# Kernel optimization log

Hardware: AMD Instinct MI355X
Metric: run time of the kernel (lower is better)

## Reference

```python
import jax, jax.numpy as jnp
import numpy as np

N = 100_000      # nodes
E = 3_200_000    # edges (avg degree 32)
F_IN = 100       # raw feature dim (embedding Linear(100, 64))
H = 64           # in/hidden/out channels
C = 18           # class_num
EPS = 1e-12      # F.normalize eps


def _sage_conv(x, src, dst, edge_weight, Wl, bl, Wr):
    """PyG-style SAGEConv: mean-aggregate neighbor messages, two linears, L2 normalize."""
    msg = x[src]                                   # [E, d] gather of x_j
    if edge_weight is not None:
        msg = msg * edge_weight[:, None]
    agg = jax.ops.segment_sum(msg, dst, num_segments=N)                       # [N, d]
    deg = jax.ops.segment_sum(jnp.ones((src.shape[0],), x.dtype), dst, num_segments=N)
    mean = agg / jnp.maximum(deg, 1.0)[:, None]
    out = mean @ Wl + bl + x @ Wr                  # lin_l(aggr) + lin_r(root)
    nrm = jnp.sqrt(jnp.sum(out * out, axis=-1, keepdims=True))
    return out / jnp.maximum(nrm, EPS)


def setup_inputs() -> dict:
    key = jax.random.key(0)
    ks = jax.random.split(key, 16)
    s = 0.1
    inp = {
        "x": jax.random.normal(ks[0], (N, F_IN), jnp.float32),
        "edge_index": jax.random.randint(ks[1], (2, E), 0, N, dtype=jnp.int64),
        "edge_weight": jax.random.uniform(ks[2], (E,), jnp.float32),
        "emb_W": jax.random.normal(ks[3], (F_IN, H), jnp.float32) * s,
        "emb_b": jnp.zeros((H,), jnp.float32),
    }
    k = 4
    for i in (1, 2, 3):
        inp[f"Wl{i}"] = jax.random.normal(ks[k], (H, H), jnp.float32) * s; k += 1
        inp[f"bl{i}"] = jnp.zeros((H,), jnp.float32)
        inp[f"Wr{i}"] = jax.random.normal(ks[k], (H, H), jnp.float32) * s; k += 1
    inp["Wl4"] = jax.random.normal(ks[k], (H, C), jnp.float32) * s; k += 1
    inp["bl4"] = jnp.zeros((C,), jnp.float32)
    inp["Wr4"] = jax.random.normal(ks[k], (H, C), jnp.float32) * s
    return inp


def reference(x, edge_index, edge_weight, emb_W, emb_b,
              Wl1, bl1, Wr1, Wl2, bl2, Wr2, Wl3, bl3, Wr3,
              Wl4, bl4, Wr4):
    src, dst = edge_index[0], edge_index[1]
    h = jax.nn.relu(x @ emb_W + emb_b)             # embedding MLP
    for Wl, bl, Wr in ((Wl1, bl1, Wr1), (Wl2, bl2, Wr2), (Wl3, bl3, Wr3)):
        h = jax.nn.relu(_sage_conv(h, src, dst, edge_weight, Wl, bl, Wr))
        # dropout p=0.2 is identity in eval mode
    return _sage_conv(h, src, dst, None, Wl4, bl4, Wr4)
```

## Files before the change

kernel.cpp:

```cpp
#include <hip/hip_runtime.h>
#include <hip/hip_bf16.h>

#define N_NODES   100000
#define N_EDGES   3200000
#define F_IN      100
#define H_DIM     64
#define C_NUM     18
#define NPB       256
#define N_BKT     391
#define EPB       8192
#define N_TILES   1563

typedef __attribute__((ext_vector_type(8))) short short8;
typedef __attribute__((ext_vector_type(4))) float f32x4;
typedef __attribute__((ext_vector_type(2))) float f32x2;

__device__ __forceinline__ float ldf(const void* p, long long i, int isbf) {
    if (isbf) return __bfloat162float(((const __hip_bfloat16*)p)[i]);
    return ((const float*)p)[i];
}
__device__ __forceinline__ int ldi(const void* p, long long i, int is64) {
    if (is64) return (int)(((const long long*)p)[i]);
    return ((const int*)p)[i];
}
__device__ __forceinline__ unsigned short f2us(float f) {
    __hip_bfloat16 b = __float2bfloat16(f);
    return *(unsigned short*)&b;
}
__device__ __forceinline__ unsigned char f2fp8(float f) {
    int p = __builtin_amdgcn_cvt_pk_fp8_f32(f, 0.0f, 0, false);
    return (unsigned char)(p & 0xFF);
}

__global__ void detect_kernel(const void* ei, const void* x, int* flags)
{
    if (blockIdx.x != 0 || threadIdx.x >= 64) return;
    const int lane = threadIdx.x;
    const long long* e64 = (const long long*)ei;
    int bad = 0;
#pragma unroll
    for (int i = lane; i < 128; i += 64) {
        long long v = e64[i];
        if (v < 0 || v >= N_NODES) bad = 1;
    }
    unsigned long long anybad = __ballot(bad);
    const __hip_bfloat16* xb = (const __hip_bfloat16*)x;
    int cnt = 0;
#pragma unroll
    for (int i = lane; i < 256; i += 64) {
        float v = fabsf(__bfloat162float(xb[i]));
        if (v == 0.0f || (v > 9.5367431640625e-7f && v < 1.0e6f)) ++cnt;
    }
#pragma unroll
    for (int m = 1; m <= 32; m <<= 1) cnt += __shfl_xor(cnt, m);
    if (lane == 0) {
        flags[0] = (anybad == 0ULL) ? 1 : 0;
        flags[1] = (cnt >= 240) ? 1 : 0;
    }
}

__global__ void zero_cnt(int* __restrict__ pcnt)
{
    int i = threadIdx.x;
    if (i < N_BKT) pcnt[i] = 0;
}

__global__ __launch_bounds__(1024) void radix_count(const void* ei, int* __restrict__ pcnt,
                                                    const int* __restrict__ flags)
{
    __shared__ int hist[N_BKT];
    const int t = threadIdx.x;
    if (t < N_BKT) hist[t] = 0;
    __syncthreads();
    const int base = blockIdx.x * EPB;
    const int n = min(EPB, N_EDGES - base);
    const int is64 = flags[0];
    for (int j = t; j < n; j += 1024) {
        int d = ldi(ei, (long long)N_EDGES + base + j, is64);
        atomicAdd(&hist[d >> 8], 1);
    }
    __syncthreads();
    if (t < N_BKT) atomicAdd(&pcnt[t], hist[t]);
}

__global__ void scan_bkt(const int* __restrict__ cnt, int* __restrict__ base,
                         int* __restrict__ cursor)
{
    __shared__ int tmp[512];
    const int t = threadIdx.x;
    int v = (t < N_BKT) ? cnt[t] : 0;
    tmp[t] = v;
    __syncthreads();
    for (int off = 1; off < 512; off <<= 1) {
        int add = (t >= off) ? tmp[t - off] : 0;
        __syncthreads();
        tmp[t] += add;
        __syncthreads();
    }
    if (t < N_BKT) { base[t] = tmp[t] - v; cursor[t] = tmp[t] - v; }
    if (t == 511) base[N_BKT] = tmp[511];
}

__global__ __launch_bounds__(1024) void radix_scatter(const void* ei, const void* ew,
                                                      int* __restrict__ gcursor,
                                                      uint2* __restrict__ temp,
                                                      const int* __restrict__ flags)
{
    __shared__ uint2 stage[EPB];
    __shared__ int hist[512], scan_s[512];
    __shared__ int gbase[N_BKT], lcur[N_BKT];
    const int t = threadIdx.x;
    if (t < 512) hist[t] = 0;
    __syncthreads();

    const int base = blockIdx.x * EPB;
    const int n = min(EPB, N_EDGES - base);
    const int is64 = flags[0], isbf = flags[1];

    int  bkt[8];
    uint2 pk[8];
#pragma unroll
    for (int j = 0; j < 8; ++j) {
        int i = j * 1024 + t;
        bkt[j] = -1;
        if (i < n) {
            int e = base + i;
            int s = ldi(ei, e, is64);
            int d = ldi(ei, (long long)N_EDGES + e, is64);
            float w = ldf(ew, e, isbf);
            bkt[j] = d >> 8;
            pk[j].x = (unsigned)s | ((unsigned)(d & (NPB - 1)) << 17);
            pk[j].y = (unsigned)f2us(w) | ((unsigned)bkt[j] << 16);
            atomicAdd(&hist[bkt[j]], 1);
        }
    }
    __syncthreads();
    if (t < 512) scan_s[t] = hist[t];
    __syncthreads();
    for (int off = 1; off < 512; off <<= 1) {
        int add = 0;
        if (t < 512 && t >= off) add = scan_s[t - off];
        __syncthreads();
        if (t < 512) scan_s[t] += add;
        __syncthreads();
    }
    if (t < N_BKT) {
        int excl = scan_s[t] - hist[t];
        lcur[t] = excl;
        gbase[t] = atomicAdd(&gcursor[t], hist[t]) - excl;
    }
    __syncthreads();
#pragma unroll
    for (int j = 0; j < 8; ++j) {
        if (bkt[j] >= 0) {
            int pos = atomicAdd(&lcur[bkt[j]], 1);
            stage[pos] = pk[j];
        }
    }
    __syncthreads();
#pragma unroll
    for (int j = 0; j < 8; ++j) {
        int i = j * 1024 + t;
        if (i < n) {
            int b = (int)(stage[i].y >> 16);
            temp[gbase[b] + i] = stage[i];
        }
    }
}

__global__ __launch_bounds__(256) void csr_build(const uint2* __restrict__ temp,
                          const int* __restrict__ pbase,
                          unsigned int* __restrict__ csr_pk,
                          int* __restrict__ deg, int* __restrict__ row_start,
                          float* __restrict__ inv_deg)
{
    __shared__ int cnt[NPB], scan_s[NPB], cur[NPB];
    const int b = blockIdx.x;
    const int t = threadIdx.x;
    cnt[t] = 0;
    __syncthreads();
    const int bs = pbase[b];
    const int be = pbase[b + 1];
    for (int i = bs + t; i < be; i += NPB)
        atomicAdd(&cnt[(temp[i].x >> 17) & (NPB - 1)], 1);
    __syncthreads();
    int v = cnt[t];
    scan_s[t] = v;
    __syncthreads();
    for (int off = 1; off < NPB; off <<= 1) {
        int add = (t >= off) ? scan_s[t - off] : 0;
        __syncthreads();
        scan_s[t] += add;
        __syncthreads();
    }
    int excl = bs + scan_s[t] - v;
    cur[t] = excl;
    int node = b * NPB + t;
    if (node < N_NODES) {
        deg[node]       = v;
        row_start[node] = excl;
        inv_deg[node]   = 1.0f / (float)max(v, 1);
    }
    __syncthreads();
    for (int i = bs + t; i < be; i += NPB) {
        uint2 e = temp[i];
        int k = (e.x >> 17) & (NPB - 1);
        int pos = atomicAdd(&cur[k], 1);
        csr_pk[pos] = (e.x & 0x1FFFFu) | ((e.y & 0x7FFFu) << 17);
    }
}

template <int CP, int COUT>
__device__ __forceinline__ void stage_W(unsigned short* W_s, const void* Wl, const void* Wr,
                                        int t, int isbf)
{
    constexpr int KP = 136;
    const int n0 = t >> 3, k8a = t & 7;
    for (int n = n0; n < CP; n += 32) {
#pragma unroll
        for (int hh = 0; hh < 2; ++hh) {
            int k8 = k8a + hh * 8;
            union { unsigned short u[8]; short8 v; } tmp;
#pragma unroll
            for (int j = 0; j < 8; ++j) {
                int k = k8 * 8 + j;
                float val = 0.0f;
                if (n < COUT && k < 128)
                    val = (k < 64) ? ldf(Wl, (long long)k * COUT + n, isbf)
                                   : ldf(Wr, (long long)(k - 64) * COUT + n, isbf);
                tmp.u[j] = f2us(val);
            }
            *(short8*)&W_s[n * KP + k8 * 8] = tmp.v;
        }
    }
}

__global__ void embed_mfma(const void* x, const void* W, const void* b,
                           __hip_bfloat16* __restrict__ h,
                           unsigned char* __restrict__ h8,
                           const int* __restrict__ flags)
{
    constexpr int KP = 136;
    __shared__ unsigned short W_s[H_DIM * KP];
    __shared__ unsigned short x_s[64 * KP];
    __shared__ float b_s[H_DIM];
    const int t = threadIdx.x;
    const int isbf = flags[1];

    {
        const int n0 = t >> 3, k8a = t & 7;
        for (int n = n0; n < H_DIM; n += 32) {
#pragma unroll
            for (int hh = 0; hh < 2; ++hh) {
                int k8 = k8a + hh * 8;
                union { unsigned short u[8]; short8 v; } tmp;
#pragma unroll
                for (int j = 0; j < 8; ++j) {
                    int k = k8 * 8 + j;
                    tmp.u[j] = (k < F_IN) ? f2us(ldf(W, (long long)k * H_DIM + n, isbf))
                                          : (unsigned short)0;
                }
                *(short8*)&W_s[n * KP + k8 * 8] = tmp.v;
            }
        }
    }
    if (t < H_DIM) b_s[t] = ldf(b, t, isbf);
    for (int i = t; i < 64 * 36; i += 256) {
        int row = i / 36, col = 100 + (i % 36);
        x_s[row * KP + col] = 0;
    }

    const int wave = t >> 6, lane = t & 63, c = lane & 15, quad = lane >> 4;

    for (int tile = blockIdx.x; tile < N_TILES; tile += gridDim.x) {
        const int nb0 = tile * 64;
        const int valid = min(64, N_NODES - nb0);
        __syncthreads();
        if (isbf) {
            const uint2* xu = (const uint2*)x + (size_t)nb0 * 25;
            for (int i2 = t; i2 < valid * 25; i2 += 256) {
                int row = i2 / 25, col4 = i2 - row * 25;
                *(uint2*)&x_s[row * KP + col4 * 4] = xu[i2];
            }
        } else {
            for (int i = t; i < valid * 100; i += 256) {
                int row = i / 100, col = i - row * 100;
                x_s[row * KP + col] = f2us(((const float*)x)[(size_t)(nb0 + row) * 100 + col]);
            }
        }
        if (valid < 64) {
            for (int i = t; i < (64 - valid) * 100; i += 256) {
                int row = valid + i / 100, col = i % 100;
                x_s[row * KP + col] = 0;
            }
        }
        __syncthreads();

        short8 bfrag[4][4];
#pragma unroll
        for (int nt = 0; nt < 4; ++nt)
#pragma unroll
            for (int kt = 0; kt < 4; ++kt)
                bfrag[nt][kt] = *(const short8*)&W_s[(nt * 16 + c) * KP + kt * 32 + quad * 8];

        short8 afrag[4];
#pragma unroll
        for (int kt = 0; kt < 4; ++kt)
            afrag[kt] = *(const short8*)&x_s[(wave * 16 + c) * KP + kt * 32 + quad * 8];

        f32x4 acc[4] = {};
#pragma unroll
        for (int nt = 0; nt < 4; ++nt)
#pragma unroll
            for (int kt = 0; kt < 4; ++kt)
                acc[nt] = __builtin_amdgcn_mfma_f32_16x16x32_bf16(afrag[kt], bfrag[nt][kt], acc[nt], 0, 0, 0);

        const int nb = nb0 + wave * 16;
#pragma unroll
        for (int nt = 0; nt < 4; ++nt)
#pragma unroll
            for (int reg = 0; reg < 4; ++reg) {
                int nn = nb + quad * 4 + reg;
                int col = nt * 16 + c;
                if (nn < N_NODES) {
                    float v = fmaxf(acc[nt][reg] + b_s[col], 0.0f);
                    h[(size_t)nn * H_DIM + col] = __float2bfloat16(v);
                    h8[(size_t)nn * H_DIM + col] = f2fp8(v);
                }
            }
    }
}

#define ACC16(HV, W) do {                                                          \
    f32x2 f_;                                                                      \
    f_ = __builtin_amdgcn_cvt_pk_f32_fp8((int)HV.x, false); a[0]=fmaf(W,f_.x,a[0]);  a[1]=fmaf(W,f_.y,a[1]);   \
    f_ = __builtin_amdgcn_cvt_pk_f32_fp8((int)HV.x, true ); a[2]=fmaf(W,f_.x,a[2]);  a[3]=fmaf(W,f_.y,a[3]);   \
    f_ = __builtin_amdgcn_cvt_pk_f32_fp8((int)HV.y, false); a[4]=fmaf(W,f_.x,a[4]);  a[5]=fmaf(W,f_.y,a[5]);   \
    f_ = __builtin_amdgcn_cvt_pk_f32_fp8((int)HV.y, true ); a[6]=fmaf(W,f_.x,a[6]);  a[7]=fmaf(W,f_.y,a[7]);   \
    f_ = __builtin_amdgcn_cvt_pk_f32_fp8((int)HV.z, false); a[8]=fmaf(W,f_.x,a[8]);  a[9]=fmaf(W,f_.y,a[9]);   \
    f_ = __builtin_amdgcn_cvt_pk_f32_fp8((int)HV.z, true ); a[10]=fmaf(W,f_.x,a[10]); a[11]=fmaf(W,f_.y,a[11]); \
    f_ = __builtin_amdgcn_cvt_pk_f32_fp8((int)HV.w, false); a[12]=fmaf(W,f_.x,a[12]); a[13]=fmaf(W,f_.y,a[13]); \
    f_ = __builtin_amdgcn_cvt_pk_f32_fp8((int)HV.w, true ); a[14]=fmaf(W,f_.x,a[14]); a[15]=fmaf(W,f_.y,a[15]); \
} while (0)

template <bool USE_W>
__global__ __launch_bounds__(256) void gather_mean(const unsigned char* __restrict__ h8,
                            const unsigned int* __restrict__ csr_pk,
                            const int* __restrict__ row_start,
                            const int* __restrict__ deg,
                            const float* __restrict__ inv_deg,
                            __hip_bfloat16* __restrict__ mean)
{
    const int lane = threadIdx.x & 63;
    const int c4 = lane & 3;
    const int r4 = lane >> 2;
    const int wid = blockIdx.x * 4 + (threadIdx.x >> 6);
    const int nw  = gridDim.x * 4;

    for (int n = wid; n < N_NODES; n += nw) {
        const int s0 = row_start[n];
        const int d0 = deg[n];
        unsigned int ev = (lane < d0) ? csr_pk[s0 + lane] : 0u;
        const int m0 = min(d0, 64);
        float a[16] = {};

        for (int j0 = 0; j0 < m0; j0 += 32) {
            unsigned int eA = __shfl(ev, j0 + r4);
            unsigned int eB = __shfl(ev, j0 + 16 + r4);
            uint4 hvA = *(const uint4*)(h8 + (size_t)(eA & 0x1FFFF) * H_DIM + 16 * c4);
            uint4 hvB = *(const uint4*)(h8 + (size_t)(eB & 0x1FFFF) * H_DIM + 16 * c4);
            float wA, wB;
            if (USE_W) {
                wA = __uint_as_float((eA & 0xFFFE0000u) >> 1);
                wB = __uint_as_float((eB & 0xFFFE0000u) >> 1);
            } else {
                wA = (j0 + r4 < m0) ? 1.0f : 0.0f;
                wB = (j0 + 16 + r4 < m0) ? 1.0f : 0.0f;
            }
            ACC16(hvA, wA);
            ACC16(hvB, wB);
        }
        for (int jb = 64; jb < d0; jb += 16) {
            int j = jb + r4;
            unsigned int e2 = (j < d0) ? csr_pk[s0 + j] : 0u;
            float w;
            if (USE_W) w = __uint_as_float((e2 & 0xFFFE0000u) >> 1);
            else       w = (j < d0) ? 1.0f : 0.0f;
            uint4 hv = *(const uint4*)(h8 + (size_t)(e2 & 0x1FFFF) * H_DIM + 16 * c4);
            ACC16(hv, w);
        }

#pragma unroll
        for (int i = 0; i < 8; ++i) {
            float keep = (lane & 4) ? a[i + 8] : a[i];
            float give = (lane & 4) ? a[i] : a[i + 8];
            a[i] = keep + __shfl_xor(give, 4);
        }
#pragma unroll
        for (int i = 0; i < 4; ++i) {
            float keep = (lane & 8) ? a[i + 4] : a[i];
            float give = (lane & 8) ? a[i] : a[i + 4];
            a[i] = keep + __shfl_xor(give, 8);
        }
#pragma unroll
        for (int i = 0; i < 2; ++i) {
            float keep = (lane & 16) ? a[i + 2] : a[i];
            float give = (lane & 16) ? a[i] : a[i + 2];
            a[i] = keep + __shfl_xor(give, 16);
        }
        {
            float keep = (lane & 32) ? a[1] : a[0];
            float give = (lane & 32) ? a[0] : a[1];
            a[0] = keep + __shfl_xor(give, 32);
        }
        const int f = c4 * 16 + ((lane >> 2) & 1) * 8 + ((lane >> 3) & 1) * 4
                    + ((lane >> 4) & 1) * 2 + ((lane >> 5) & 1);
        mean[(size_t)n * H_DIM + f] = __float2bfloat16(a[0] * inv_deg[n]);
    }
}

template <int COUT, bool RELU, bool FINAL>
__global__ void transform_mfma(const __hip_bfloat16* __restrict__ meanp,
                               const __hip_bfloat16* __restrict__ hp,
                               const void* Wl, const void* bl, const void* Wr,
                               __hip_bfloat16* __restrict__ h_out,
                               unsigned char* __restrict__ h8_out,
                               const int* __restrict__ flags, void* dout)
{
    constexpr int CP = (COUT + 15) & ~15;
    constexpr int NT = CP / 16;
    constexpr int KP = 136;
    __shared__ unsigned short W_s[CP * KP];
    __shared__ float b_s[CP];
    const int t = threadIdx.x;
    const int isbf = flags[1];
    stage_W<CP, COUT>(W_s, Wl, Wr, t, isbf);
    if (t < CP) b_s[t] = (t < COUT) ? ldf(bl, t, isbf) : 0.0f;
    __syncthreads();

    const int wave = t >> 6, lane = t & 63, c = lane & 15, quad = lane >> 4;
    short8 bfrag[NT][4];
#pragma unroll
    for (int nt = 0; nt < NT; ++nt)
#pragma unroll
        for (int kt = 0; kt < 4; ++kt)
            bfrag[nt][kt] = *(const short8*)&W_s[(nt * 16 + c) * KP + kt * 32 + quad * 8];

    for (int tile = blockIdx.x; tile < N_TILES; tile += gridDim.x) {
        const int nbw = tile * 64 + wave * 16;
        if (nbw >= N_NODES) continue;
        int node = nbw + c; if (node >= N_NODES) node = N_NODES - 1;

        short8 afrag[4];
#pragma unroll
        for (int kt = 0; kt < 4; ++kt) {
            const __hip_bfloat16* sp = (kt < 2) ? meanp : hp;
            afrag[kt] = *(const short8*)(sp + (size_t)node * H_DIM + (kt & 1) * 32 + quad * 8);
        }

        f32x4 acc[NT] = {};
#pragma unroll
        for (int nt = 0; nt < NT; ++nt)
#pragma unroll
            for (int kt = 0; kt < 4; ++kt)
                acc[nt] = __builtin_amdgcn_mfma_f32_16x16x32_bf16(afrag[kt], bfrag[nt][kt], acc[nt], 0, 0, 0);

        float rs[4];
#pragma unroll
        for (int reg = 0; reg < 4; ++reg) {
            float s2 = 0.f;
#pragma unroll
            for (int nt = 0; nt < NT; ++nt) {
                float v = acc[nt][reg] + b_s[nt * 16 + c];
                acc[nt][reg] = v;
                s2 += v * v;
            }
            s2 += __shfl_xor(s2, 1); s2 += __shfl_xor(s2, 2);
            s2 += __shfl_xor(s2, 4); s2 += __shfl_xor(s2, 8);
            rs[reg] = 1.0f / fmaxf(sqrtf(s2), 1e-12f);
        }

#pragma unroll
        for (int nt = 0; nt < NT; ++nt)
#pragma unroll
            for (int reg = 0; reg < 4; ++reg) {
                int nn  = nbw + quad * 4 + reg;
                int col = nt * 16 + c;
                if (nn < N_NODES && col < COUT) {
                    float v = acc[nt][reg] * rs[reg];
                    if (RELU) v = fmaxf(v, 0.0f);
                    if (FINAL) {
                        if (isbf) ((__hip_bfloat16*)dout)[(size_t)nn * COUT + col] = __float2bfloat16(v);
                        else      ((float*)dout)[(size_t)nn * COUT + col] = v;
                    } else {
                        h_out[(size_t)nn * H_DIM + col] = __float2bfloat16(v);
                        h8_out[(size_t)nn * H_DIM + col] = f2fp8(v);
                    }
                }
            }
    }
}

extern "C" void kernel_launch(void* const* d_in, const int* in_sizes, int n_in,
                              void* d_out, int out_size, void* d_ws, size_t ws_size,
                              hipStream_t stream)
{
    const void* x    = d_in[0];
    const void* ei   = d_in[1];
    const void* ew   = d_in[2];
    const void* embW = d_in[3];
    const void* embB = d_in[4];
    const void* Wl1 = d_in[5];  const void* bl1 = d_in[6];  const void* Wr1 = d_in[7];
    const void* Wl2 = d_in[8];  const void* bl2 = d_in[9];  const void* Wr2 = d_in[10];
    const void* Wl3 = d_in[11]; const void* bl3 = d_in[12]; const void* Wr3 = d_in[13];
    const void* Wl4 = d_in[14]; const void* bl4 = d_in[15]; const void* Wr4 = d_in[16];
    (void)in_sizes; (void)n_in; (void)out_size; (void)ws_size;

    char* ws = (char*)d_ws;
    size_t off = 0;
    auto alloc = [&](size_t bytes) -> void* {
        void* p = ws + off;
        off += (bytes + 255) & ~(size_t)255;
        return p;
    };
    uint2* temp = (uint2*)alloc((size_t)N_EDGES * sizeof(uint2));
    __hip_bfloat16* hA = (__hip_bfloat16*)temp;
    __hip_bfloat16* hB = (__hip_bfloat16*)((char*)temp + (size_t)N_NODES * H_DIM * 2);
    unsigned int* csr_pk = (unsigned int*)alloc((size_t)N_EDGES * sizeof(unsigned int));
    __hip_bfloat16* mn = (__hip_bfloat16*)alloc((size_t)N_NODES * H_DIM * 2);
    unsigned char* h8 = (unsigned char*)alloc((size_t)N_NODES * H_DIM);
    int*   pcnt    = (int*)  alloc((N_BKT)     * sizeof(int));
    int*   pbase   = (int*)  alloc((N_BKT + 1) * sizeof(int));
    int*   pcursor = (int*)  alloc((N_BKT)     * sizeof(int));
    int*   deg     = (int*)  alloc((size_t)N_NODES * sizeof(int));
    int*   row_st  = (int*)  alloc((size_t)N_NODES * sizeof(int));
    float* inv_deg = (float*)alloc((size_t)N_NODES * sizeof(float));
    int*   flags   = (int*)  alloc(256);

    const int NBr = (N_EDGES + EPB - 1) / EPB;

    detect_kernel<<<1, 64, 0, stream>>>(ei, x, flags);
    zero_cnt<<<1, 512, 0, stream>>>(pcnt);
    radix_count<<<NBr, 1024, 0, stream>>>(ei, pcnt, flags);
    scan_bkt<<<1, 512, 0, stream>>>(pcnt, pbase, pcursor);
    radix_scatter<<<NBr, 1024, 0, stream>>>(ei, ew, pcursor, temp, flags);
    csr_build<<<N_BKT, NPB, 0, stream>>>(temp, pbase, csr_pk, deg, row_st, inv_deg);

    embed_mfma<<<512, 256, 0, stream>>>(x, embW, embB, hA, h8, flags);

    gather_mean<true><<<2048, 256, 0, stream>>>(h8, csr_pk, row_st, deg, inv_deg, mn);
    transform_mfma<H_DIM, true, false><<<512, 256, 0, stream>>>(
        mn, hA, Wl1, bl1, Wr1, hB, h8, flags, d_out);
    gather_mean<true><<<2048, 256, 0, stream>>>(h8, csr_pk, row_st, deg, inv_deg, mn);
    transform_mfma<H_DIM, true, false><<<512, 256, 0, stream>>>(
        mn, hB, Wl2, bl2, Wr2, hA, h8, flags, d_out);
    gather_mean<true><<<2048, 256, 0, stream>>>(h8, csr_pk, row_st, deg, inv_deg, mn);
    transform_mfma<H_DIM, true, false><<<512, 256, 0, stream>>>(
        mn, hA, Wl3, bl3, Wr3, hB, h8, flags, d_out);
    gather_mean<false><<<2048, 256, 0, stream>>>(h8, csr_pk, row_st, deg, inv_deg, mn);
    transform_mfma<C_NUM, false, true><<<512, 256, 0, stream>>>(
        mn, hB, Wl4, bl4, Wr4, nullptr, nullptr, flags, d_out);
}
```

Measured before the change: 520.6 us.

## Retune radix buckets, fold zeroing into detect, double-buffer fp8 features, grow grids

Halves nodes per bucket (782 buckets of 128 nodes) and halves edges per scatter block so the scatter kernel uses less LDS and runs more blocks. The pcnt zeroing moves into detect_kernel, removing one launch, and int64 indices are read as their low 32-bit word. The fp8 feature buffer is split into two ping-pong buffers, so a transform kernel no longer overwrites the buffer the previous gather read. Transform kernels launch one block per tile instead of 512 blocks. Together these trade a larger scan and more, smaller CSR-build blocks for better occupancy in the preprocessing and transform stages.

Result: no change. 527.3 us (+1.3%).

```diff
diff --git a/kernel.cpp b/kernel.cpp
--- a/kernel.cpp
+++ b/kernel.cpp
@@ -6,9 +6,10 @@
 #define F_IN      100
 #define H_DIM     64
 #define C_NUM     18
-#define NPB       256
-#define N_BKT     391
-#define EPB       8192
+#define NPB       128
+#define N_BKT     782
+#define EPB_C     8192
+#define EPB_S     4096
 #define N_TILES   1563
 
 typedef __attribute__((ext_vector_type(8))) short short8;
@@ -19,8 +20,8 @@
     if (isbf) return __bfloat162float(((const __hip_bfloat16*)p)[i]);
     return ((const float*)p)[i];
 }
-__device__ __forceinline__ int ldi(const void* p, long long i, int is64) {
-    if (is64) return (int)(((const long long*)p)[i]);
+__device__ __forceinline__ int ldi_lo(const void* p, long long i, int is64) {
+    if (is64) return ((const int*)p)[2 * i];
     return ((const int*)p)[i];
 }
 __device__ __forceinline__ unsigned short f2us(float f) {
@@ -32,10 +33,13 @@
     return (unsigned char)(p & 0xFF);
 }
 
-__global__ void detect_kernel(const void* ei, const void* x, int* flags)
-{
-    if (blockIdx.x != 0 || threadIdx.x >= 64) return;
-    const int lane = threadIdx.x;
+__global__ void detect_kernel(const void* ei, const void* x, int* flags,
+                              int* __restrict__ pcnt)
+{
+    const int t = threadIdx.x;
+    for (int i = t; i < N_BKT; i += 256) pcnt[i] = 0;
+    if (t >= 64) return;
+    const int lane = t;
     const long long* e64 = (const long long*)ei;
     int bad = 0;
 #pragma unroll
@@ -59,12 +63,6 @@
     }
 }
 
-__global__ void zero_cnt(int* __restrict__ pcnt)
-{
-    int i = threadIdx.x;
-    if (i < N_BKT) pcnt[i] = 0;
-}
-
 __global__ __launch_bounds__(1024) void radix_count(const void* ei, int* __restrict__ pcnt,
                                                     const int* __restrict__ flags)
 {
@@ -72,33 +70,34 @@
     const int t = threadIdx.x;
     if (t < N_BKT) hist[t] = 0;
     __syncthreads();
-    const int base = blockIdx.x * EPB;
-    const int n = min(EPB, N_EDGES - base);
+    const int base = blockIdx.x * EPB_C;
+    const int n = min(EPB_C, N_EDGES - base);
     const int is64 = flags[0];
     for (int j = t; j < n; j += 1024) {
-        int d = ldi(ei, (long long)N_EDGES + base + j, is64);
-        atomicAdd(&hist[d >> 8], 1);
+        int d = ldi_lo(ei, (long long)N_EDGES + base + j, is64);
+        atomicAdd(&hist[d >> 7], 1);
     }
     __syncthreads();
     if (t < N_BKT) atomicAdd(&pcnt[t], hist[t]);
 }
 
-__global__ void scan_bkt(const int* __restrict__ cnt, int* __restrict__ base,
-                         int* __restrict__ cursor)
-{
-    __shared__ int tmp[512];
+__global__ __launch_bounds__(1024) void scan_bkt(const int* __restrict__ cnt,
+                                                 int* __restrict__ base,
+                                                 int* __restrict__ cursor)
+{
+    __shared__ int tmp[1024];
     const int t = threadIdx.x;
     int v = (t < N_BKT) ? cnt[t] : 0;
     tmp[t] = v;
     __syncthreads();
-    for (int off = 1; off < 512; off <<= 1) {
+    for (int off = 1; off < 1024; off <<= 1) {
         int add = (t >= off) ? tmp[t - off] : 0;
         __syncthreads();
         tmp[t] += add;
         __syncthreads();
     }
     if (t < N_BKT) { base[t] = tmp[t] - v; cursor[t] = tmp[t] - v; }
-    if (t == 511) base[N_BKT] = tmp[511];
+    if (t == 1023) base[N_BKT] = tmp[1023];
 }
 
 __global__ __launch_bounds__(1024) void radix_scatter(const void* ei, const void* ew,
@@ -106,42 +105,41 @@
                                                       uint2* __restrict__ temp,
                                                       const int* __restrict__ flags)
 {
-    __shared__ uint2 stage[EPB];
-    __shared__ int hist[512], scan_s[512];
+    __shared__ uint2 stage[EPB_S];
+    __shared__ int hist[1024], scan_s[1024];
     __shared__ int gbase[N_BKT], lcur[N_BKT];
     const int t = threadIdx.x;
-    if (t < 512) hist[t] = 0;
-    __syncthreads();
-
-    const int base = blockIdx.x * EPB;
-    const int n = min(EPB, N_EDGES - base);
+    hist[t] = 0;
+    __syncthreads();
+
+    const int base = blockIdx.x * EPB_S;
+    const int n = min(EPB_S, N_EDGES - base);
     const int is64 = flags[0], isbf = flags[1];
 
-    int  bkt[8];
-    uint2 pk[8];
-#pragma unroll
-    for (int j = 0; j < 8; ++j) {
+    int  bkt[4];
+    uint2 pk[4];
+#pragma unroll
+    for (int j = 0; j < 4; ++j) {
         int i = j * 1024 + t;
         bkt[j] = -1;
         if (i < n) {
             int e = base + i;
-            int s = ldi(ei, e, is64);
-            int d = ldi(ei, (long long)N_EDGES + e, is64);
+            int s = ldi_lo(ei, e, is64);
+            int d = ldi_lo(ei, (long long)N_EDGES + e, is64);
             float w = ldf(ew, e, isbf);
-            bkt[j] = d >> 8;
+            bkt[j] = d >> 7;
             pk[j].x = (unsigned)s | ((unsigned)(d & (NPB - 1)) << 17);
             pk[j].y = (unsigned)f2us(w) | ((unsigned)bkt[j] << 16);
             atomicAdd(&hist[bkt[j]], 1);
         }
     }
     __syncthreads();
-    if (t < 512) scan_s[t] = hist[t];
-    __syncthreads();
-    for (int off = 1; off < 512; off <<= 1) {
-        int add = 0;
-        if (t < 512 && t >= off) add = scan_s[t - off];
-        __syncthreads();
-        if (t < 512) scan_s[t] += add;
+    scan_s[t] = hist[t];
+    __syncthreads();
+    for (int off = 1; off < 1024; off <<= 1) {
+        int add = (t >= off) ? scan_s[t - off] : 0;
+        __syncthreads();
+        scan_s[t] += add;
         __syncthreads();
     }
     if (t < N_BKT) {
@@ -151,7 +149,7 @@
     }
     __syncthreads();
 #pragma unroll
-    for (int j = 0; j < 8; ++j) {
+    for (int j = 0; j < 4; ++j) {
         if (bkt[j] >= 0) {
             int pos = atomicAdd(&lcur[bkt[j]], 1);
             stage[pos] = pk[j];
@@ -159,7 +157,7 @@
     }
     __syncthreads();
 #pragma unroll
-    for (int j = 0; j < 8; ++j) {
+    for (int j = 0; j < 4; ++j) {
         int i = j * 1024 + t;
         if (i < n) {
             int b = (int)(stage[i].y >> 16);
@@ -168,7 +166,7 @@
     }
 }
 
-__global__ __launch_bounds__(256) void csr_build(const uint2* __restrict__ temp,
+__global__ __launch_bounds__(NPB) void csr_build(const uint2* __restrict__ temp,
                           const int* __restrict__ pbase,
                           unsigned int* __restrict__ csr_pk,
                           int* __restrict__ deg, int* __restrict__ row_start,
@@ -528,7 +526,8 @@
     __hip_bfloat16* hB = (__hip_bfloat16*)((char*)temp + (size_t)N_NODES * H_DIM * 2);
     unsigned int* csr_pk = (unsigned int*)alloc((size_t)N_EDGES * sizeof(unsigned int));
     __hip_bfloat16* mn = (__hip_bfloat16*)alloc((size_t)N_NODES * H_DIM * 2);
-    unsigned char* h8 = (unsigned char*)alloc((size_t)N_NODES * H_DIM);
+    unsigned char* h8A = (unsigned char*)alloc((size_t)N_NODES * H_DIM);
+    unsigned char* h8B = (unsigned char*)alloc((size_t)N_NODES * H_DIM);
     int*   pcnt    = (int*)  alloc((N_BKT)     * sizeof(int));
     int*   pbase   = (int*)  alloc((N_BKT + 1) * sizeof(int));
     int*   pcursor = (int*)  alloc((N_BKT)     * sizeof(int));
@@ -537,27 +536,27 @@
     float* inv_deg = (float*)alloc((size_t)N_NODES * sizeof(float));
     int*   flags   = (int*)  alloc(256);
 
-    const int NBr = (N_EDGES + EPB - 1) / EPB;
-
-    detect_kernel<<<1, 64, 0, stream>>>(ei, x, flags);
-    zero_cnt<<<1, 512, 0, stream>>>(pcnt);
-    radix_count<<<NBr, 1024, 0, stream>>>(ei, pcnt, flags);
-    scan_bkt<<<1, 512, 0, stream>>>(pcnt, pbase, pcursor);
-    radix_scatter<<<NBr, 1024, 0, stream>>>(ei, ew, pcursor, temp, flags);
+    const int NBc = (N_EDGES + EPB_C - 1) / EPB_C;
+    const int NBs = (N_EDGES + EPB_S - 1) / EPB_S;
+
+    detect_kernel<<<1, 256, 0, stream>>>(ei, x, flags, pcnt);
+    radix_count<<<NBc, 1024, 0, stream>>>(ei, pcnt, flags);
+    scan_bkt<<<1, 1024, 0, stream>>>(pcnt, pbase, pcursor);
+    radix_scatter<<<NBs, 1024, 0, stream>>>(ei, ew, pcursor, temp, flags);
     csr_build<<<N_BKT, NPB, 0, stream>>>(temp, pbase, csr_pk, deg, row_st, inv_deg);
 
-    embed_mfma<<<512, 256, 0, stream>>>(x, embW, embB, hA, h8, flags);
-
-    gather_mean<true><<<2048, 256, 0, stream>>>(h8, csr_pk, row_st, deg, inv_deg, mn);
-    transform_mfma<H_DIM, true, false><<<512, 256, 0, stream>>>(
-        mn, hA, Wl1, bl1, Wr1, hB, h8, flags, d_out);
-    gather_mean<true><<<2048, 256, 0, stream>>>(h8, csr_pk, row_st, deg, inv_deg, mn);
-    transform_mfma<H_DIM, true, false><<<512, 256, 0, stream>>>(
-        mn, hB, Wl2, bl2, Wr2, hA, h8, flags, d_out);
-    gather_mean<true><<<2048, 256, 0, stream>>>(h8, csr_pk, row_st, deg, inv_deg, mn);
-    transform_mfma<H_DIM, true, false><<<512, 256, 0, stream>>>(
-        mn, hA, Wl3, bl3, Wr3, hB, h8, flags, d_out);
-    gather_mean<false><<<2048, 256, 0, stream>>>(h8, csr_pk, row_st, deg, inv_deg, mn);
-    transform_mfma<C_NUM, false, true><<<512, 256, 0, stream>>>(
+    embed_mfma<<<512, 256, 0, stream>>>(x, embW, embB, hA, h8A, flags);
+
+    gather_mean<true><<<2048, 256, 0, stream>>>(h8A, csr_pk, row_st, deg, inv_deg, mn);
+    transform_mfma<H_DIM, true, false><<<N_TILES, 256, 0, stream>>>(
+        mn, hA, Wl1, bl1, Wr1, hB, h8B, flags, d_out);
+    gather_mean<true><<<2048, 256, 0, stream>>>(h8B, csr_pk, row_st, deg, inv_deg, mn);
+    transform_mfma<H_DIM, true, false><<<N_TILES, 256, 0, stream>>>(
+        mn, hB, Wl2, bl2, Wr2, hA, h8A, flags, d_out);
+    gather_mean<true><<<2048, 256, 0, stream>>>(h8A, csr_pk, row_st, deg, inv_deg, mn);
+    transform_mfma<H_DIM, true, false><<<N_TILES, 256, 0, stream>>>(
+        mn, hA, Wl3, bl3, Wr3, hB, h8B, flags, d_out);
+    gather_mean<false><<<2048, 256, 0, stream>>>(h8B, csr_pk, row_st, deg, inv_deg, mn);
+    transform_mfma<C_NUM, false, true><<<N_TILES, 256, 0, stream>>>(
         mn, hB, Wl4, bl4, Wr4, nullptr, nullptr, flags, d_out);
 }
```
